# Performance work log

Measured on AMD Instinct MI355X. Metric: run time of the kernel, lower is better.

Reference implementation:

```python
import jax, jax.numpy as jnp
import numpy as np

UNITS = 768
OUT_STEPS = 64
INPUT_DIM = 96


def setup_inputs() -> dict:
    key = jax.random.key(0)
    ks = jax.random.split(key, 7)
    B, T = 2048, 24
    s_ih = 1.0 / np.sqrt(UNITS)
    inputs = jax.random.normal(ks[0], (B, T, INPUT_DIM), dtype=jnp.float32)
    # PyTorch LSTMCell params: weight_ih [4U, I], weight_hh [4U, U], biases [4U]
    W_ih = jax.random.uniform(ks[1], (4 * UNITS, INPUT_DIM), minval=-s_ih, maxval=s_ih, dtype=jnp.float32)
    W_hh = jax.random.uniform(ks[2], (4 * UNITS, UNITS), minval=-s_ih, maxval=s_ih, dtype=jnp.float32)
    b_ih = jax.random.uniform(ks[3], (4 * UNITS,), minval=-s_ih, maxval=s_ih, dtype=jnp.float32)
    b_hh = jax.random.uniform(ks[4], (4 * UNITS,), minval=-s_ih, maxval=s_ih, dtype=jnp.float32)
    # Dense: Linear(units, input_dim)
    s_d = 1.0 / np.sqrt(UNITS)
    W_d = jax.random.uniform(ks[5], (INPUT_DIM, UNITS), minval=-s_d, maxval=s_d, dtype=jnp.float32)
    b_d = jax.random.uniform(ks[6], (INPUT_DIM,), minval=-s_d, maxval=s_d, dtype=jnp.float32)
    return {"inputs": inputs, "W_ih": W_ih, "W_hh": W_hh, "b_ih": b_ih, "b_hh": b_hh, "W_d": W_d, "b_d": b_d}


def _lstm_cell(x, h, c, W_ih, W_hh, b_ih, b_hh):
    # gates: [B, 4U], PyTorch gate order i, f, g, o
    gates = x @ W_ih.T + b_ih + h @ W_hh.T + b_hh
    i, f, g, o = jnp.split(gates, 4, axis=-1)
    i = jax.nn.sigmoid(i)
    f = jax.nn.sigmoid(f)
    g = jnp.tanh(g)
    o = jax.nn.sigmoid(o)
    c_new = f * c + i * g
    h_new = o * jnp.tanh(c_new)
    return h_new, c_new


def reference(inputs, W_ih, W_hh, b_ih, b_hh, W_d, b_d):
    B = inputs.shape[0]
    h0 = jnp.zeros((B, UNITS), dtype=inputs.dtype)
    c0 = jnp.zeros((B, UNITS), dtype=inputs.dtype)
    # warmup: feed last timestep
    x0 = inputs[:, -1, :]
    h, c = _lstm_cell(x0, h0, c0, W_ih, W_hh, b_ih, b_hh)
    pred0 = h @ W_d.T + b_d

    def step(carry, _):
        pred, h, c = carry
        h2, c2 = _lstm_cell(pred, h, c, W_ih, W_hh, b_ih, b_hh)
        pred2 = h2 @ W_d.T + b_d
        return (pred2, h2, c2), pred2

    _, preds_rest = jax.lax.scan(step, (pred0, h, c), None, length=OUT_STEPS - 1)
    # preds_rest: [out_steps-1, B, I] -> stack with pred0 along time axis 1
    preds = jnp.concatenate([pred0[None], preds_rest], axis=0)  # [out_steps, B, I]
    return jnp.transpose(preds, (1, 0, 2))  # [B, out_steps, I]
```

## Files before the change

kernel.cpp:

```cpp
#include <hip/hip_runtime.h>
#include <hip/hip_bf16.h>
#include <stdint.h>

typedef __hip_bfloat16 bf16_t;
typedef __attribute__((ext_vector_type(4))) float f32x4;
typedef __attribute__((ext_vector_type(8))) short s16x8;

#define UNITS 768
#define NCOLS 3072
#define NPRED 96
#define NPAD  3200
#define MROWS 2048
#define BM 128
#define BN 128
#define BK 32

#define GLL16(ldsp, gp) \
  __builtin_amdgcn_global_load_lds((const __attribute__((address_space(1))) void*)(gp), \
                                   (__attribute__((address_space(3))) void*)(ldsp), 16, 0, 0)

__device__ __forceinline__ float sigf(float x) {
    return __builtin_amdgcn_rcpf(1.f + __expf(-x));
}
__device__ __forceinline__ float tanh_fast(float x) {
    return 1.f - 2.f * __builtin_amdgcn_rcpf(1.f + __expf(2.f * x));
}


__global__ void prep_b0(const float* __restrict__ W_ih, bf16_t* __restrict__ B0T) {
    int idx = blockIdx.x * 256 + threadIdx.x;
    if (idx >= NCOLS * 96) return;
    int c = idx / 96, k = idx % 96;
    int u = ((c >> 6) << 4) + (c & 15);
    int g = (c >> 4) & 3;
    B0T[idx] = (bf16_t)W_ih[(g * UNITS + u) * 96 + k];
}

__global__ void prep_x0(const float* __restrict__ inputs, bf16_t* __restrict__ x0) {
    int idx = blockIdx.x * 256 + threadIdx.x;
    int b = idx / 96, k = idx % 96;
    x0[idx] = (bf16_t)inputs[(b * 24 + 23) * 96 + k];
}

__global__ void prep_bias(const float* __restrict__ b_ih, const float* __restrict__ b_hh,
                          const float* __restrict__ W_ih, const float* __restrict__ b_d,
                          float* __restrict__ b0_r, float* __restrict__ beff_r) {
    int c = blockIdx.x * 256 + threadIdx.x;
    if (c >= NCOLS) return;
    int u = ((c >> 6) << 4) + (c & 15);
    int g = (c >> 4) & 3;
    int r = g * UNITS + u;
    float v = b_ih[r] + b_hh[r];
    float acc = 0.f;
    for (int j = 0; j < 96; ++j) acc += W_ih[r * 96 + j] * b_d[j];
    b0_r[c] = v;
    beff_r[c] = v + acc;
}

__global__ void prep_beff2(const float* __restrict__ W_hh, const float* __restrict__ W_ih,
                           const float* __restrict__ W_d, bf16_t* __restrict__ BeffT) {
    __shared__ float sWih[64][96];
    __shared__ float sWd[96][64];
    const int c0 = blockIdx.x * 64, k0 = blockIdx.y * 64;
    const int tid = threadIdx.x;
    for (int i = tid; i < 64 * 96; i += 256) {
        int cc = i / 96, j = i % 96;
        int c = c0 + cc;
        int u = ((c >> 6) << 4) + (c & 15);
        int g = (c >> 4) & 3;
        sWih[cc][j] = W_ih[(g * UNITS + u) * 96 + j];
    }
    for (int i = tid; i < 96 * 64; i += 256) {
        int j = i / 64, kk = i % 64;
        sWd[j][kk] = W_d[j * UNITS + k0 + kk];
    }
    __syncthreads();
    const int kk = tid & 63;
    const int cc0 = (tid >> 6) * 16;
    for (int cc = cc0; cc < cc0 + 16; ++cc) {
        float acc = 0.f;
#pragma unroll 12
        for (int j = 0; j < 96; ++j) acc += sWih[cc][j] * sWd[j][kk];
        int c = c0 + cc;
        int u = ((c >> 6) << 4) + (c & 15);
        int g = (c >> 4) & 3;
        int r = g * UNITS + u;
        BeffT[(size_t)c * UNITS + k0 + kk] = (bf16_t)(W_hh[(size_t)r * UNITS + k0 + kk] + acc);
    }
}

__global__ void prep_wdt(const float* __restrict__ W_d, bf16_t* __restrict__ BeffT) {
    int idx = blockIdx.x * 256 + threadIdx.x;
    int c = idx / UNITS, k = idx % UNITS;
    float v = (c < NPRED) ? W_d[c * UNITS + k] : 0.f;
    BeffT[(size_t)(NCOLS + c) * UNITS + k] = (bf16_t)v;
}

__global__ __launch_bounds__(256, 2)
void step_kernel(const bf16_t* __restrict__ A,
                 const bf16_t* __restrict__ BT,
                 const float* __restrict__ bias_r,
                 const float* __restrict__ b_d,
                 float* __restrict__ c_state,
                 bf16_t* __restrict__ h_out,
                 float* __restrict__ out,
                 int Kdim, int col_tile_base, int t, int is_first)
{
    __shared__ bf16_t sA0[BM * BK];
    __shared__ bf16_t sB0[BN * BK];
    __shared__ bf16_t sA1[BM * BK];
    __shared__ bf16_t sB1[BN * BK];

    const int tid = threadIdx.x;
    const int wave = tid >> 6;
    const int lane = tid & 63;
    const int wr = wave >> 1, wc = wave & 1;
    const int l15 = lane & 15, l4 = lane >> 4;

    const int mt = blockIdx.x;
    const int nt = col_tile_base + blockIdx.y;
    const int m0 = mt * BM;
    const int n0 = nt * BN;
    const bool is_pred = (nt >= 24);

    const int u = nt * 32 + wc * 16 + l15;
    float cold[16];
    float bi[4];
#pragma unroll
    for (int i = 0; i < 16; ++i) cold[i] = 0.f;
    if (!is_pred) {
        if (!is_first) {
#pragma unroll
            for (int i = 0; i < 4; ++i)
#pragma unroll
                for (int r = 0; r < 4; ++r)
                    cold[i * 4 + r] =
                        c_state[(size_t)(m0 + wr * 64 + i * 16 + l4 * 4 + r) * UNITS + u];
        }
#pragma unroll
        for (int f = 0; f < 4; ++f) bi[f] = bias_r[n0 + wc * 64 + f * 16 + l15];
    } else {
#pragma unroll
        for (int f = 0; f < 4; ++f) {
            int j = wc * 64 + f * 16 + l15;
            bi[f] = (j < NPRED) ? b_d[j] : 0.f;
        }
    }

    f32x4 acc[4][4];
#pragma unroll
    for (int i = 0; i < 4; ++i)
#pragma unroll
        for (int j = 0; j < 4; ++j) acc[i][j] = f32x4{0.f, 0.f, 0.f, 0.f};

    const int o0 = wave * 1024 + lane * 16;
    const int nk = Kdim >> 5;

#define STAGE(dstA, dstB, KT) do {                                                  \
        const int _k0 = (KT) << 5;                                                  \
        _Pragma("unroll")                                                           \
        for (int _r = 0; _r < 2; ++_r) {                                            \
            int _ob = o0 + _r * 4096;                                               \
            int _row = _ob >> 6;                                                    \
            int _kb = _ob & 63;                                                     \
            const bf16_t* _gA = A + (size_t)(m0 + _row) * Kdim + _k0 + (_kb >> 1);  \
            GLL16((dstA) + ((wave * 1024 + _r * 4096) >> 1), _gA);                  \
            const bf16_t* _gB = BT + (size_t)(n0 + _row) * Kdim + _k0 + (_kb >> 1); \
            GLL16((dstB) + ((wave * 1024 + _r * 4096) >> 1), _gB);                  \
        }                                                                           \
    } while (0)

    STAGE(sA0, sB0, 0);

    for (int kt = 0; kt < nk; ++kt) {
        __syncthreads();

        const char* sAc = (kt & 1) ? (const char*)sA1 : (const char*)sA0;
        const char* sBc = (kt & 1) ? (const char*)sB1 : (const char*)sB0;

        s16x8 af[4], bfr[4];
#pragma unroll
        for (int f = 0; f < 4; ++f) {
            af[f]  = *(const s16x8*)(sAc + (wr * 64 + f * 16 + l15) * 64 + l4 * 16);
            bfr[f] = *(const s16x8*)(sBc + (wc * 64 + f * 16 + l15) * 64 + l4 * 16);
        }

        if (kt + 1 < nk) {
            if (kt & 1) { STAGE(sA0, sB0, kt + 1); }
            else        { STAGE(sA1, sB1, kt + 1); }
        }

#pragma unroll
        for (int i = 0; i < 4; ++i)
#pragma unroll
            for (int j = 0; j < 4; ++j)
                acc[i][j] = __builtin_amdgcn_mfma_f32_16x16x32_bf16(af[i], bfr[j], acc[i][j], 0, 0, 0);
    }
#undef STAGE

    if (!is_pred) {
#pragma unroll
        for (int i = 0; i < 4; ++i) {
#pragma unroll
            for (int r = 0; r < 4; ++r) {
                int row = m0 + wr * 64 + i * 16 + l4 * 4 + r;
                float gi = acc[i][0][r] + bi[0];
                float gf = acc[i][1][r] + bi[1];
                float gg = acc[i][2][r] + bi[2];
                float go = acc[i][3][r] + bi[3];
                float si = sigf(gi);
                float sf = sigf(gf);
                float tg = tanh_fast(gg);
                float so = sigf(go);
                size_t cidx = (size_t)row * UNITS + u;
                float cn = sf * cold[i * 4 + r] + si * tg;
                c_state[cidx] = cn;
                h_out[cidx] = (bf16_t)(so * tanh_fast(cn));
            }
        }
    } else {
#pragma unroll
        for (int f = 0; f < 4; ++f) {
            int j = wc * 64 + f * 16 + l15;
            if (j < NPRED) {
#pragma unroll
                for (int i = 0; i < 4; ++i)
#pragma unroll
                    for (int r = 0; r < 4; ++r) {
                        int row = m0 + wr * 64 + i * 16 + l4 * 4 + r;
                        out[((size_t)row * 64 + (t - 1)) * NPRED + j] = acc[i][f][r] + bi[f];
                    }
            }
        }
    }
}

extern "C" void kernel_launch(void* const* d_in, const int* in_sizes, int n_in,
                              void* d_out, int out_size, void* d_ws, size_t ws_size,
                              hipStream_t stream)
{
    const float* inputs = (const float*)d_in[0];
    const float* W_ih   = (const float*)d_in[1];
    const float* W_hh   = (const float*)d_in[2];
    const float* b_ih   = (const float*)d_in[3];
    const float* b_hh   = (const float*)d_in[4];
    const float* W_d    = (const float*)d_in[5];
    const float* b_d    = (const float*)d_in[6];
    float* out = (float*)d_out;

    char* ws = (char*)d_ws;
    size_t off = 0;
    auto alloc = [&](size_t bytes) -> char* {
        char* p = ws + off;
        off = (off + bytes + 255) & ~(size_t)255;
        return p;
    };
    bf16_t* B0T   = (bf16_t*)alloc((size_t)NCOLS * 96 * 2);
    bf16_t* BeffT = (bf16_t*)alloc((size_t)NPAD * UNITS * 2);
    bf16_t* x0    = (bf16_t*)alloc((size_t)MROWS * 96 * 2);
    bf16_t* h0    = (bf16_t*)alloc((size_t)MROWS * UNITS * 2);
    bf16_t* h1    = (bf16_t*)alloc((size_t)MROWS * UNITS * 2);
    float*  cst   = (float*)alloc((size_t)MROWS * UNITS * 4);
    float*  b0r   = (float*)alloc(NCOLS * 4);
    float*  beffr = (float*)alloc(NCOLS * 4);

    prep_b0   <<<(NCOLS * 96 + 255) / 256, 256, 0, stream>>>(W_ih, B0T);
    prep_x0   <<<(MROWS * 96) / 256, 256, 0, stream>>>(inputs, x0);
    prep_bias <<<(NCOLS + 255) / 256, 256, 0, stream>>>(b_ih, b_hh, W_ih, b_d, b0r, beffr);
    prep_beff2<<<dim3(48, 12), 256, 0, stream>>>(W_hh, W_ih, W_d, BeffT);
    prep_wdt  <<<(128 * UNITS) / 256, 256, 0, stream>>>(W_d, BeffT);

    bf16_t* h[2] = {h0, h1};

    step_kernel<<<dim3(16, 24), 256, 0, stream>>>(x0, B0T, b0r, b_d, cst, h[1], out,
                                                  96, 0, 0, 1);
    for (int n = 1; n < 64; ++n)
        step_kernel<<<dim3(16, 25), 256, 0, stream>>>(h[n & 1], BeffT, beffr, b_d, cst,
                                                      h[(n + 1) & 1], out, UNITS, 0, n, 0);
    step_kernel<<<dim3(16, 1), 256, 0, stream>>>(h[0], BeffT, beffr, b_d, cst, h[1], out,
                                                 UNITS, 24, 64, 0);
    (void)ws_size; (void)in_sizes; (void)n_in; (void)out_size;
}
```

Before: 1.353 ms.

## Deepen LDS pipeline to 4 stages, XCD-aware block swizzle, tile-local cell state layout

Replaces the double-buffered K loop with a 4-buffer pipeline: three tiles are prefetched, and each iteration waits on vmcnt plus a raw barrier instead of a full syncthreads. The grid becomes 1D with a swizzle that maps consecutive blocks across the 8 XCDs. Cell state is stored in a per-tile, per-lane layout so it is read and written with vectorized f32x4 accesses instead of strided scalar ones. The goal is to hide global load latency and cut uncoalesced c_state traffic, at the cost of more LDS per block (64KB) and redundant clamped loads at the tail.

```diff
diff --git a/kernel.cpp b/kernel.cpp
--- a/kernel.cpp
+++ b/kernel.cpp
@@ -9,11 +9,12 @@
 #define UNITS 768
 #define NCOLS 3072
 #define NPRED 96
-#define NPAD  3200
 #define MROWS 2048
 #define BM 128
 #define BN 128
 #define BK 32
+
+#define WAIT_VMCNT8 0xF78
 
 #define GLL16(ldsp, gp) \
   __builtin_amdgcn_global_load_lds((const __attribute__((address_space(1))) void*)(gp), \
@@ -104,12 +105,9 @@
                  float* __restrict__ c_state,
                  bf16_t* __restrict__ h_out,
                  float* __restrict__ out,
-                 int Kdim, int col_tile_base, int t, int is_first)
+                 int Kdim, int nt_off, int t, int is_first)
 {
-    __shared__ bf16_t sA0[BM * BK];
-    __shared__ bf16_t sB0[BN * BK];
-    __shared__ bf16_t sA1[BM * BK];
-    __shared__ bf16_t sB1[BN * BK];
+    __shared__ bf16_t sAll[4][2][BM * BK];
 
     const int tid = threadIdx.x;
     const int wave = tid >> 6;
@@ -117,25 +115,25 @@
     const int wr = wave >> 1, wc = wave & 1;
     const int l15 = lane & 15, l4 = lane >> 4;
 
-    const int mt = blockIdx.x;
-    const int nt = col_tile_base + blockIdx.y;
+    const int per = gridDim.x >> 3;
+    const int g = (blockIdx.x & 7) * per + (blockIdx.x >> 3);
+    const int nt = nt_off + (g >> 4);
+    const int mt = g & 15;
     const int m0 = mt * BM;
     const int n0 = nt * BN;
     const bool is_pred = (nt >= 24);
 
     const int u = nt * 32 + wc * 16 + l15;
-    float cold[16];
+    const int slot = nt * 16 + mt;
+    float* cbase = c_state + (((size_t)slot * 4 + wave) * 64 + lane) * 16;
+    f32x4 cold4[4];
     float bi[4];
 #pragma unroll
-    for (int i = 0; i < 16; ++i) cold[i] = 0.f;
+    for (int q = 0; q < 4; ++q) cold4[q] = f32x4{0.f, 0.f, 0.f, 0.f};
     if (!is_pred) {
         if (!is_first) {
 #pragma unroll
-            for (int i = 0; i < 4; ++i)
-#pragma unroll
-                for (int r = 0; r < 4; ++r)
-                    cold[i * 4 + r] =
-                        c_state[(size_t)(m0 + wr * 64 + i * 16 + l4 * 4 + r) * UNITS + u];
+            for (int q = 0; q < 4; ++q) cold4[q] = *(const f32x4*)(cbase + q * 4);
         }
 #pragma unroll
         for (int f = 0; f < 4; ++f) bi[f] = bias_r[n0 + wc * 64 + f * 16 + l15];
@@ -146,6 +144,7 @@
             bi[f] = (j < NPRED) ? b_d[j] : 0.f;
         }
     }
+    asm volatile("" ::: "memory");
 
     f32x4 acc[4][4];
 #pragma unroll
@@ -156,27 +155,35 @@
     const int o0 = wave * 1024 + lane * 16;
     const int nk = Kdim >> 5;
 
-#define STAGE(dstA, dstB, KT) do {                                                  \
-        const int _k0 = (KT) << 5;                                                  \
+#define STAGE(BUF, KT) do {                                                         \
+        const int _kt = ((KT) < nk) ? (KT) : (nk - 1);                              \
+        const int _k0 = _kt << 5;                                                   \
+        bf16_t* _dA = &sAll[(BUF)][0][0];                                           \
+        bf16_t* _dB = &sAll[(BUF)][1][0];                                           \
         _Pragma("unroll")                                                           \
         for (int _r = 0; _r < 2; ++_r) {                                            \
             int _ob = o0 + _r * 4096;                                               \
             int _row = _ob >> 6;                                                    \
             int _kb = _ob & 63;                                                     \
             const bf16_t* _gA = A + (size_t)(m0 + _row) * Kdim + _k0 + (_kb >> 1);  \
-            GLL16((dstA) + ((wave * 1024 + _r * 4096) >> 1), _gA);                  \
+            GLL16(_dA + ((wave * 1024 + _r * 4096) >> 1), _gA);                     \
             const bf16_t* _gB = BT + (size_t)(n0 + _row) * Kdim + _k0 + (_kb >> 1); \
-            GLL16((dstB) + ((wave * 1024 + _r * 4096) >> 1), _gB);                  \
+            GLL16(_dB + ((wave * 1024 + _r * 4096) >> 1), _gB);                     \
         }                                                                           \
     } while (0)
 
-    STAGE(sA0, sB0, 0);
+    STAGE(0, 0);
+    STAGE(1, 1);
+    STAGE(2, 2);
 
     for (int kt = 0; kt < nk; ++kt) {
-        __syncthreads();
-
-        const char* sAc = (kt & 1) ? (const char*)sA1 : (const char*)sA0;
-        const char* sBc = (kt & 1) ? (const char*)sB1 : (const char*)sB0;
+        __builtin_amdgcn_s_waitcnt(WAIT_VMCNT8);
+        __builtin_amdgcn_s_barrier();
+        asm volatile("" ::: "memory");
+
+        const int cb = kt & 3;
+        const char* sAc = (const char*)&sAll[cb][0][0];
+        const char* sBc = (const char*)&sAll[cb][1][0];
 
         s16x8 af[4], bfr[4];
 #pragma unroll
@@ -185,10 +192,7 @@
             bfr[f] = *(const s16x8*)(sBc + (wc * 64 + f * 16 + l15) * 64 + l4 * 16);
         }
 
-        if (kt + 1 < nk) {
-            if (kt & 1) { STAGE(sA0, sB0, kt + 1); }
-            else        { STAGE(sA1, sB1, kt + 1); }
-        }
+        STAGE((kt + 3) & 3, kt + 3);
 
 #pragma unroll
         for (int i = 0; i < 4; ++i)
@@ -199,6 +203,7 @@
 #undef STAGE
 
     if (!is_pred) {
+        f32x4 cnew4[4];
 #pragma unroll
         for (int i = 0; i < 4; ++i) {
 #pragma unroll
@@ -212,12 +217,13 @@
                 float sf = sigf(gf);
                 float tg = tanh_fast(gg);
                 float so = sigf(go);
-                size_t cidx = (size_t)row * UNITS + u;
-                float cn = sf * cold[i * 4 + r] + si * tg;
-                c_state[cidx] = cn;
-                h_out[cidx] = (bf16_t)(so * tanh_fast(cn));
+                float cn = sf * cold4[i][r] + si * tg;
+                cnew4[i][r] = cn;
+                h_out[(size_t)row * UNITS + u] = (bf16_t)(so * tanh_fast(cn));
             }
         }
+#pragma unroll
+        for (int q = 0; q < 4; ++q) *(f32x4*)(cbase + q * 4) = cnew4[q];
     } else {
 #pragma unroll
         for (int f = 0; f < 4; ++f) {
@@ -256,7 +262,7 @@
         return p;
     };
     bf16_t* B0T   = (bf16_t*)alloc((size_t)NCOLS * 96 * 2);
-    bf16_t* BeffT = (bf16_t*)alloc((size_t)NPAD * UNITS * 2);
+    bf16_t* BeffT = (bf16_t*)alloc((size_t)3200 * UNITS * 2);
     bf16_t* x0    = (bf16_t*)alloc((size_t)MROWS * 96 * 2);
     bf16_t* h0    = (bf16_t*)alloc((size_t)MROWS * UNITS * 2);
     bf16_t* h1    = (bf16_t*)alloc((size_t)MROWS * UNITS * 2);
@@ -272,12 +278,11 @@
 
     bf16_t* h[2] = {h0, h1};
 
-    step_kernel<<<dim3(16, 24), 256, 0, stream>>>(x0, B0T, b0r, b_d, cst, h[1], out,
-                                                  96, 0, 0, 1);
+    step_kernel<<<384, 256, 0, stream>>>(x0, B0T, b0r, b_d, cst, h[1], out, 96, 0, 0, 1);
     for (int n = 1; n < 64; ++n)
-        step_kernel<<<dim3(16, 25), 256, 0, stream>>>(h[n & 1], BeffT, beffr, b_d, cst,
-                                                      h[(n + 1) & 1], out, UNITS, 0, n, 0);
-    step_kernel<<<dim3(16, 1), 256, 0, stream>>>(h[0], BeffT, beffr, b_d, cst, h[1], out,
-                                                 UNITS, 24, 64, 0);
+        step_kernel<<<400, 256, 0, stream>>>(h[n & 1], BeffT, beffr, b_d, cst,
+                                             h[(n + 1) & 1], out, UNITS, 0, n, 0);
+    step_kernel<<<16, 256, 0, stream>>>(h[0], BeffT, beffr, b_d, cst, h[1], out,
+                                        UNITS, 24, 64, 0);
     (void)ws_size; (void)in_sizes; (void)n_in; (void)out_size;
 }
```

After: 1.407 ms. 4.0% more time.

## Halve M tile, remap blocks XCD-aware, and store cell state in fragment order

Applied to the files above, without the earlier changes.

The row tile drops from 128 to 64, so each step launches 800 blocks instead of 400. Launch bounds rise to 4 blocks per SIMD for better occupancy and wave balance across the CUs. Blocks are remapped with a stride-8 swizzle so that neighbouring tiles land on the same XCD for L2 reuse of the weight tiles. Cell state now lives in a per-thread fragment-order layout read and written as two float4 vectors, and the c-state load moves after the first stage prefetch to overlap with it. The cost is more A/B staging overhead per FLOP, because each B tile is now loaded twice as often across M.

```diff
diff --git a/kernel.cpp b/kernel.cpp
--- a/kernel.cpp
+++ b/kernel.cpp
@@ -9,11 +9,11 @@
 #define UNITS 768
 #define NCOLS 3072
 #define NPRED 96
-#define NPAD  3200
 #define MROWS 2048
-#define BM 128
+#define BM 64
 #define BN 128
 #define BK 32
+#define NMT 32
 
 #define GLL16(ldsp, gp) \
   __builtin_amdgcn_global_load_lds((const __attribute__((address_space(1))) void*)(gp), \
@@ -96,7 +96,7 @@
     BeffT[(size_t)(NCOLS + c) * UNITS + k] = (bf16_t)v;
 }
 
-__global__ __launch_bounds__(256, 2)
+__global__ __launch_bounds__(256, 4)
 void step_kernel(const bf16_t* __restrict__ A,
                  const bf16_t* __restrict__ BT,
                  const float* __restrict__ bias_r,
@@ -104,7 +104,7 @@
                  float* __restrict__ c_state,
                  bf16_t* __restrict__ h_out,
                  float* __restrict__ out,
-                 int Kdim, int col_tile_base, int t, int is_first)
+                 int Kdim, int nt_off, int t, int is_first)
 {
     __shared__ bf16_t sA0[BM * BK];
     __shared__ bf16_t sB0[BN * BK];
@@ -117,54 +117,30 @@
     const int wr = wave >> 1, wc = wave & 1;
     const int l15 = lane & 15, l4 = lane >> 4;
 
-    const int mt = blockIdx.x;
-    const int nt = col_tile_base + blockIdx.y;
+    const int per = gridDim.x >> 3;
+    const int g = (blockIdx.x & 7) * per + (blockIdx.x >> 3);
+    const int nt = nt_off + (g >> 5);
+    const int mt = g & 31;
     const int m0 = mt * BM;
     const int n0 = nt * BN;
     const bool is_pred = (nt >= 24);
 
-    const int u = nt * 32 + wc * 16 + l15;
-    float cold[16];
-    float bi[4];
-#pragma unroll
-    for (int i = 0; i < 16; ++i) cold[i] = 0.f;
-    if (!is_pred) {
-        if (!is_first) {
-#pragma unroll
-            for (int i = 0; i < 4; ++i)
-#pragma unroll
-                for (int r = 0; r < 4; ++r)
-                    cold[i * 4 + r] =
-                        c_state[(size_t)(m0 + wr * 64 + i * 16 + l4 * 4 + r) * UNITS + u];
-        }
-#pragma unroll
-        for (int f = 0; f < 4; ++f) bi[f] = bias_r[n0 + wc * 64 + f * 16 + l15];
-    } else {
-#pragma unroll
-        for (int f = 0; f < 4; ++f) {
-            int j = wc * 64 + f * 16 + l15;
-            bi[f] = (j < NPRED) ? b_d[j] : 0.f;
-        }
-    }
-
-    f32x4 acc[4][4];
-#pragma unroll
-    for (int i = 0; i < 4; ++i)
-#pragma unroll
-        for (int j = 0; j < 4; ++j) acc[i][j] = f32x4{0.f, 0.f, 0.f, 0.f};
-
     const int o0 = wave * 1024 + lane * 16;
     const int nk = Kdim >> 5;
 
 #define STAGE(dstA, dstB, KT) do {                                                  \
         const int _k0 = (KT) << 5;                                                  \
+        {                                                                           \
+            int _row = o0 >> 6;                                                     \
+            int _kb = o0 & 63;                                                      \
+            const bf16_t* _gA = A + (size_t)(m0 + _row) * Kdim + _k0 + (_kb >> 1);  \
+            GLL16((dstA) + ((wave * 1024) >> 1), _gA);                              \
+        }                                                                           \
         _Pragma("unroll")                                                           \
         for (int _r = 0; _r < 2; ++_r) {                                            \
             int _ob = o0 + _r * 4096;                                               \
             int _row = _ob >> 6;                                                    \
             int _kb = _ob & 63;                                                     \
-            const bf16_t* _gA = A + (size_t)(m0 + _row) * Kdim + _k0 + (_kb >> 1);  \
-            GLL16((dstA) + ((wave * 1024 + _r * 4096) >> 1), _gA);                  \
             const bf16_t* _gB = BT + (size_t)(n0 + _row) * Kdim + _k0 + (_kb >> 1); \
             GLL16((dstB) + ((wave * 1024 + _r * 4096) >> 1), _gB);                  \
         }                                                                           \
@@ -172,18 +148,47 @@
 
     STAGE(sA0, sB0, 0);
 
+    const int u = nt * 32 + wc * 16 + l15;
+    const int slot = nt * NMT + mt;
+    float* cbase = c_state + (((size_t)slot * 4 + wave) * 64 + lane) * 8;
+    f32x4 cold4[2];
+    float bi[4];
+    cold4[0] = f32x4{0.f, 0.f, 0.f, 0.f};
+    cold4[1] = f32x4{0.f, 0.f, 0.f, 0.f};
+    if (!is_pred) {
+        if (!is_first) {
+            cold4[0] = *(const f32x4*)(cbase);
+            cold4[1] = *(const f32x4*)(cbase + 4);
+        }
+#pragma unroll
+        for (int f = 0; f < 4; ++f) bi[f] = bias_r[n0 + wc * 64 + f * 16 + l15];
+    } else {
+#pragma unroll
+        for (int f = 0; f < 4; ++f) {
+            int j = wc * 64 + f * 16 + l15;
+            bi[f] = (j < NPRED) ? b_d[j] : 0.f;
+        }
+    }
+
+    f32x4 acc[2][4];
+#pragma unroll
+    for (int i = 0; i < 2; ++i)
+#pragma unroll
+        for (int j = 0; j < 4; ++j) acc[i][j] = f32x4{0.f, 0.f, 0.f, 0.f};
+
     for (int kt = 0; kt < nk; ++kt) {
         __syncthreads();
 
         const char* sAc = (kt & 1) ? (const char*)sA1 : (const char*)sA0;
         const char* sBc = (kt & 1) ? (const char*)sB1 : (const char*)sB0;
 
-        s16x8 af[4], bfr[4];
-#pragma unroll
-        for (int f = 0; f < 4; ++f) {
-            af[f]  = *(const s16x8*)(sAc + (wr * 64 + f * 16 + l15) * 64 + l4 * 16);
+        s16x8 af[2], bfr[4];
+#pragma unroll
+        for (int i = 0; i < 2; ++i)
+            af[i]  = *(const s16x8*)(sAc + (wr * 32 + i * 16 + l15) * 64 + l4 * 16);
+#pragma unroll
+        for (int f = 0; f < 4; ++f)
             bfr[f] = *(const s16x8*)(sBc + (wc * 64 + f * 16 + l15) * 64 + l4 * 16);
-        }
 
         if (kt + 1 < nk) {
             if (kt & 1) { STAGE(sA0, sB0, kt + 1); }
@@ -191,7 +196,7 @@
         }
 
 #pragma unroll
-        for (int i = 0; i < 4; ++i)
+        for (int i = 0; i < 2; ++i)
 #pragma unroll
             for (int j = 0; j < 4; ++j)
                 acc[i][j] = __builtin_amdgcn_mfma_f32_16x16x32_bf16(af[i], bfr[j], acc[i][j], 0, 0, 0);
@@ -199,11 +204,12 @@
 #undef STAGE
 
     if (!is_pred) {
-#pragma unroll
-        for (int i = 0; i < 4; ++i) {
+        f32x4 cnew4[2];
+#pragma unroll
+        for (int i = 0; i < 2; ++i) {
 #pragma unroll
             for (int r = 0; r < 4; ++r) {
-                int row = m0 + wr * 64 + i * 16 + l4 * 4 + r;
+                int row = m0 + wr * 32 + i * 16 + l4 * 4 + r;
                 float gi = acc[i][0][r] + bi[0];
                 float gf = acc[i][1][r] + bi[1];
                 float gg = acc[i][2][r] + bi[2];
@@ -212,22 +218,23 @@
                 float sf = sigf(gf);
                 float tg = tanh_fast(gg);
                 float so = sigf(go);
-                size_t cidx = (size_t)row * UNITS + u;
-                float cn = sf * cold[i * 4 + r] + si * tg;
-                c_state[cidx] = cn;
-                h_out[cidx] = (bf16_t)(so * tanh_fast(cn));
+                float cn = sf * cold4[i][r] + si * tg;
+                cnew4[i][r] = cn;
+                h_out[(size_t)row * UNITS + u] = (bf16_t)(so * tanh_fast(cn));
             }
         }
+        *(f32x4*)(cbase)     = cnew4[0];
+        *(f32x4*)(cbase + 4) = cnew4[1];
     } else {
 #pragma unroll
         for (int f = 0; f < 4; ++f) {
             int j = wc * 64 + f * 16 + l15;
             if (j < NPRED) {
 #pragma unroll
-                for (int i = 0; i < 4; ++i)
+                for (int i = 0; i < 2; ++i)
 #pragma unroll
                     for (int r = 0; r < 4; ++r) {
-                        int row = m0 + wr * 64 + i * 16 + l4 * 4 + r;
+                        int row = m0 + wr * 32 + i * 16 + l4 * 4 + r;
                         out[((size_t)row * 64 + (t - 1)) * NPRED + j] = acc[i][f][r] + bi[f];
                     }
             }
@@ -256,11 +263,11 @@
         return p;
     };
     bf16_t* B0T   = (bf16_t*)alloc((size_t)NCOLS * 96 * 2);
-    bf16_t* BeffT = (bf16_t*)alloc((size_t)NPAD * UNITS * 2);
+    bf16_t* BeffT = (bf16_t*)alloc((size_t)3200 * UNITS * 2);
     bf16_t* x0    = (bf16_t*)alloc((size_t)MROWS * 96 * 2);
     bf16_t* h0    = (bf16_t*)alloc((size_t)MROWS * UNITS * 2);
     bf16_t* h1    = (bf16_t*)alloc((size_t)MROWS * UNITS * 2);
-    float*  cst   = (float*)alloc((size_t)MROWS * UNITS * 4);
+    float*  cst   = (float*)alloc((size_t)800 * 4 * 64 * 8 * 4);
     float*  b0r   = (float*)alloc(NCOLS * 4);
     float*  beffr = (float*)alloc(NCOLS * 4);
 
@@ -272,12 +279,11 @@
 
     bf16_t* h[2] = {h0, h1};
 
-    step_kernel<<<dim3(16, 24), 256, 0, stream>>>(x0, B0T, b0r, b_d, cst, h[1], out,
-                                                  96, 0, 0, 1);
+    step_kernel<<<768, 256, 0, stream>>>(x0, B0T, b0r, b_d, cst, h[1], out, 96, 0, 0, 1);
     for (int n = 1; n < 64; ++n)
-        step_kernel<<<dim3(16, 25), 256, 0, stream>>>(h[n & 1], BeffT, beffr, b_d, cst,
-                                                      h[(n + 1) & 1], out, UNITS, 0, n, 0);
-    step_kernel<<<dim3(16, 1), 256, 0, stream>>>(h[0], BeffT, beffr, b_d, cst, h[1], out,
-                                                 UNITS, 24, 64, 0);
+        step_kernel<<<800, 256, 0, stream>>>(h[n & 1], BeffT, beffr, b_d, cst,
+                                             h[(n + 1) & 1], out, UNITS, 0, n, 0);
+    step_kernel<<<32, 256, 0, stream>>>(h[0], BeffT, beffr, b_d, cst, h[1], out,
+                                        UNITS, 24, 64, 0);
     (void)ws_size; (void)in_sizes; (void)n_in; (void)out_size;
 }
```

After: 1.539 ms. 13.8% more time.
